# Kernel tuning notes

Hardware: AMD Instinct MI355X
Metric: run time of the kernel (lower is better)

The kernel has to match this reference:

```python
import jax, jax.numpy as jnp
import numpy as np

N_NODES = 10000
N_EDGES = 320000
IN_CH = 128
HID = 64
HEADS = 8
OUT_CH = 2
NEG_SLOPE = 0.2  # PyG GATConv default
EPS = 1e-16      # PyG softmax denominator eps


def setup_inputs() -> dict:
    key = jax.random.key(0)
    ks = jax.random.split(key, 12)
    x = jax.random.normal(ks[0], (N_NODES, IN_CH), dtype=jnp.float32)
    edge_index = jax.random.randint(ks[1], (2, N_EDGES), 0, N_NODES, dtype=jnp.int64)
    s = 0.05
    W1 = jax.random.normal(ks[2], (IN_CH, HEADS * HID), dtype=jnp.float32) * s
    a_src1 = jax.random.normal(ks[3], (HEADS, HID), dtype=jnp.float32) * s
    a_dst1 = jax.random.normal(ks[4], (HEADS, HID), dtype=jnp.float32) * s
    b1 = jnp.zeros((HEADS * HID,), dtype=jnp.float32)
    W2 = jax.random.normal(ks[5], (HEADS * HID, HID), dtype=jnp.float32) * s
    a_src2 = jax.random.normal(ks[6], (1, HID), dtype=jnp.float32) * s
    a_dst2 = jax.random.normal(ks[7], (1, HID), dtype=jnp.float32) * s
    b2 = jnp.zeros((HID,), dtype=jnp.float32)
    Wc = jax.random.normal(ks[8], (HID, OUT_CH), dtype=jnp.float32) * s
    bc = jnp.zeros((OUT_CH,), dtype=jnp.float32)
    return dict(x=x, edge_index=edge_index, W1=W1, a_src1=a_src1, a_dst1=a_dst1,
                b1=b1, W2=W2, a_src2=a_src2, a_dst2=a_dst2, b2=b2, Wc=Wc, bc=bc)


def gat_layer(x, src, dst, W, a_src, a_dst, bias, heads, ch, concat):
    # x: [N, F_in]; src/dst: [E] (self-loops already appended)
    N = x.shape[0]
    h = (x @ W).reshape(N, heads, ch)                 # [N, H, C]
    e_src = jnp.einsum('nhc,hc->nh', h, a_src)        # [N, H]
    e_dst = jnp.einsum('nhc,hc->nh', h, a_dst)
    e = jax.nn.leaky_relu(e_src[src] + e_dst[dst], NEG_SLOPE)  # [E, H]
    # segment softmax over destination nodes (max-shift has zero gradient)
    m = jax.lax.stop_gradient(jax.ops.segment_max(e, dst, num_segments=N))
    w = jnp.exp(e - m[dst])
    denom = jax.ops.segment_sum(w, dst, num_segments=N)
    alpha = w / (denom[dst] + EPS)                    # [E, H]
    # scatter-aggregate weighted source features
    out = jax.ops.segment_sum(h[src] * alpha[:, :, None], dst, num_segments=N)  # [N,H,C]
    out = out.reshape(N, heads * ch) if concat else out.mean(axis=1)
    return out + bias


def reference(x, edge_index, W1, a_src1, a_dst1, b1, W2, a_src2, a_dst2, b2, Wc, bc):
    N = x.shape[0]
    loop = jnp.arange(N, dtype=edge_index.dtype)
    src = jnp.concatenate([edge_index[0], loop])  # PyG add_self_loops=True
    dst = jnp.concatenate([edge_index[1], loop])
    h1 = gat_layer(x, src, dst, W1, a_src1, a_dst1, b1, HEADS, HID, True)
    h1 = jax.nn.elu(h1)
    # dropout is identity in eval mode
    h2 = gat_layer(h1, src, dst, W2, a_src2, a_dst2, b2, 1, HID, False)
    return h2 @ Wc + bc  # [N, 2]
```

## Files before the change

### kernel.cpp

```cpp
#include <hip/hip_runtime.h>
#include <hip/hip_bf16.h>

#define N_NODES 10000
#define N_EDGES 320000
#define IN_CH 128
#define HID 64
#define HEADS 8
#define OUT_CH 2
#define BM 64
#define BCAP 128
#define MPAD 10048
#define AGG1_BLKS 2048
#define AGG2_BLKS 832

typedef __attribute__((ext_vector_type(8))) short frag8;
typedef __attribute__((ext_vector_type(4))) float f32x4;

__device__ __forceinline__ unsigned short f2bf(float f) {
    union { float f; unsigned u; } v; v.f = f;
    unsigned r = (v.u + 0x7FFFu + ((v.u >> 16) & 1u)) >> 16;
    return (unsigned short)r;
}

__device__ __forceinline__ void g2l16(const void* g, void* l) {
    __builtin_amdgcn_global_load_lds(
        (__attribute__((address_space(1))) unsigned int*)g,
        (__attribute__((address_space(3))) unsigned int*)l, 16, 0, 0);
}

__global__ __launch_bounds__(256) void prep_split(
    const float* __restrict__ x, const float* __restrict__ W1,
    const float* __restrict__ W2,
    unsigned short* __restrict__ xh, unsigned short* __restrict__ xl,
    unsigned short* __restrict__ w1h, unsigned short* __restrict__ w1l,
    unsigned short* __restrict__ w2h, unsigned short* __restrict__ w2l,
    int* __restrict__ cursor) {
    int bx = blockIdx.x, tid = threadIdx.x;
    if (bx < 628) {
        int idx = bx * 256 + tid;
        int row = idx >> 4, c = idx & 15;
        float f[8];
        if (row < N_NODES) {
            float4 v0 = *(const float4*)&x[(size_t)row * IN_CH + c * 8];
            float4 v1 = *(const float4*)&x[(size_t)row * IN_CH + c * 8 + 4];
            f[0] = v0.x; f[1] = v0.y; f[2] = v0.z; f[3] = v0.w;
            f[4] = v1.x; f[5] = v1.y; f[6] = v1.z; f[7] = v1.w;
        } else {
            #pragma unroll
            for (int j = 0; j < 8; j++) f[j] = 0.f;
        }
        unsigned short hb[8], lb[8];
        #pragma unroll
        for (int j = 0; j < 8; j++) {
            hb[j] = f2bf(f[j]);
            float hf = __uint_as_float((unsigned)hb[j] << 16);
            lb[j] = f2bf(f[j] - hf);
        }
        size_t o = ((size_t)row * 16 + (c ^ (row & 15))) * 8;
        *(ushort4*)&xh[o]     = make_ushort4(hb[0], hb[1], hb[2], hb[3]);
        *(ushort4*)&xh[o + 4] = make_ushort4(hb[4], hb[5], hb[6], hb[7]);
        *(ushort4*)&xl[o]     = make_ushort4(lb[0], lb[1], lb[2], lb[3]);
        *(ushort4*)&xl[o + 4] = make_ushort4(lb[4], lb[5], lb[6], lb[7]);
    } else if (bx < 660) {
        int idx = (bx - 628) * 256 + tid;
        int kb = idx >> 9, c = idx & 511;
        int hh = c >> 6, cc = c & 63;
        unsigned short hb[8], lb[8];
        #pragma unroll
        for (int i = 0; i < 8; i++) {
            float v = W1[(size_t)(kb * 8 + i) * (HEADS * HID) + c];
            hb[i] = f2bf(v);
            float hf = __uint_as_float((unsigned)hb[i] << 16);
            lb[i] = f2bf(v - hf);
        }
        size_t o = (((size_t)hh * 16 + kb) * 64 + cc) * 8;
        *(ushort4*)&w1h[o]     = make_ushort4(hb[0], hb[1], hb[2], hb[3]);
        *(ushort4*)&w1h[o + 4] = make_ushort4(hb[4], hb[5], hb[6], hb[7]);
        *(ushort4*)&w1l[o]     = make_ushort4(lb[0], lb[1], lb[2], lb[3]);
        *(ushort4*)&w1l[o + 4] = make_ushort4(lb[4], lb[5], lb[6], lb[7]);
    } else if (bx < 676) {
        int idx = (bx - 660) * 256 + tid;
        int kb = idx >> 6, c = idx & 63;
        unsigned short hb[8], lb[8];
        #pragma unroll
        for (int i = 0; i < 8; i++) {
            float v = W2[(size_t)(kb * 8 + i) * 64 + c];
            hb[i] = f2bf(v);
            float hf = __uint_as_float((unsigned)hb[i] << 16);
            lb[i] = f2bf(v - hf);
        }
        size_t o = ((size_t)kb * 64 + c) * 8;
        *(ushort4*)&w2h[o]     = make_ushort4(hb[0], hb[1], hb[2], hb[3]);
        *(ushort4*)&w2h[o + 4] = make_ushort4(hb[4], hb[5], hb[6], hb[7]);
        *(ushort4*)&w2l[o]     = make_ushort4(lb[0], lb[1], lb[2], lb[3]);
        *(ushort4*)&w2l[o + 4] = make_ushort4(lb[4], lb[5], lb[6], lb[7]);
    } else {
        int idx = (bx - 676) * 256 + tid;
        if (idx < 2500) *(int4*)&cursor[idx * 4] = make_int4(0, 0, 0, 0);
    }
}

__global__ __launch_bounds__(256) void gemm1_mfma(
    const unsigned short* __restrict__ xh, const unsigned short* __restrict__ xl,
    const unsigned short* __restrict__ w1h, const unsigned short* __restrict__ w1l,
    const float* __restrict__ a_src1, const float* __restrict__ a_dst1,
    unsigned short* __restrict__ hfeatP,
    float* __restrict__ esAll, float* __restrict__ edAll, int M) {
    __shared__ alignas(16) unsigned short Ah[8192];
    __shared__ alignas(16) unsigned short Al[8192];
    __shared__ alignas(16) unsigned short Bh[8192];
    __shared__ alignas(16) unsigned short Bl[8192];
    int tid = threadIdx.x;
    int lane = tid & 63, w = tid >> 6;
    int vb = (blockIdx.x & 7) * 157 + (blockIdx.x >> 3);
    int h  = vb & 7;
    int bm = (vb >> 3) * BM;

    {
        const unsigned short* gAh = xh  + (size_t)bm * 128;
        const unsigned short* gAl = xl  + (size_t)bm * 128;
        const unsigned short* gBh = w1h + (size_t)h * 8192;
        const unsigned short* gBl = w1l + (size_t)h * 8192;
        #pragma unroll
        for (int i = 0; i < 4; i++) {
            int s = w * 4 + i;
            int go = s * 512 + lane * 8;
            g2l16(gAh + go, &Ah[s * 512]);
            g2l16(gAl + go, &Al[s * 512]);
            g2l16(gBh + go, &Bh[s * 512]);
            g2l16(gBl + go, &Bl[s * 512]);
        }
    }
    __syncthreads();

    int col = lane & 15, g4 = lane >> 4;
    int arow = w * 16 + col;
    f32x4 acc[4] = {};
    #pragma unroll
    for (int ks = 0; ks < 4; ks++) {
        int ai = (arow * 16 + ((ks * 4 + g4) ^ col)) * 8;
        frag8 ah = *(const frag8*)&Ah[ai];
        frag8 al = *(const frag8*)&Al[ai];
        #pragma unroll
        for (int ct = 0; ct < 4; ct++) {
            int bi = ((ks * 4 + g4) * 64 + ct * 16 + col) * 8;
            frag8 bhv = *(const frag8*)&Bh[bi];
            frag8 blv = *(const frag8*)&Bl[bi];
            acc[ct] = __builtin_amdgcn_mfma_f32_16x16x32_bf16(ah, bhv, acc[ct], 0, 0, 0);
            acc[ct] = __builtin_amdgcn_mfma_f32_16x16x32_bf16(al, bhv, acc[ct], 0, 0, 0);
            acc[ct] = __builtin_amdgcn_mfma_f32_16x16x32_bf16(ah, blv, acc[ct], 0, 0, 0);
        }
    }

    float asv[4], adv[4];
    #pragma unroll
    for (int ct = 0; ct < 4; ct++) {
        asv[ct] = a_src1[h * 64 + ct * 16 + col];
        adv[ct] = a_dst1[h * 64 + ct * 16 + col];
    }
    #pragma unroll
    for (int r = 0; r < 4; r++) {
        float s = 0.f, d = 0.f;
        #pragma unroll
        for (int ct = 0; ct < 4; ct++) {
            s += acc[ct][r] * asv[ct];
            d += acc[ct][r] * adv[ct];
        }
        #pragma unroll
        for (int off = 1; off < 16; off <<= 1) {
            s += __shfl_xor(s, off, 64);
            d += __shfl_xor(d, off, 64);
        }
        if (col == 0) {
            int gr = bm + w * 16 + g4 * 4 + r;
            if (gr < M) {
                esAll[(size_t)h * M + gr] = s;
                edAll[(size_t)h * M + gr] = d;
            }
        }
    }

    __syncthreads();
    unsigned short* Tr = Ah;
    int wrow = w * 16 + g4 * 4;
    #pragma unroll
    for (int ct = 0; ct < 4; ct++)
        #pragma unroll
        for (int r = 0; r < 4; r++)
            Tr[(wrow + r) * 68 + ct * 16 + col] = f2bf(acc[ct][r]);
    __syncthreads();
    int row = tid >> 2, q = tid & 3;
    int gr = bm + row;
    if (gr < M) {
        int tb = row * 68 + q * 16;
        ushort4 t0 = *(const ushort4*)&Tr[tb];
        ushort4 t1 = *(const ushort4*)&Tr[tb + 4];
        ushort4 t2 = *(const ushort4*)&Tr[tb + 8];
        ushort4 t3 = *(const ushort4*)&Tr[tb + 12];
        unsigned short* dst =
            &hfeatP[(((size_t)(h >> 1) * M + gr) * 128) + (h & 1) * 64 + q * 16];
        *(ushort4*)&dst[0]  = t0;
        *(ushort4*)&dst[4]  = t1;
        *(ushort4*)&dst[8]  = t2;
        *(ushort4*)&dst[12] = t3;
    }
}

__global__ void fill_bucket(const int* __restrict__ src,
                            const int* __restrict__ dst, int E,
                            int* cursor, int* __restrict__ bucket) {
    int i = blockIdx.x * blockDim.x + threadIdx.x;
    if (i < E) {
        int d = dst[i];
        int pos = atomicAdd(&cursor[d], 1);
        bucket[(d << 7) + min(pos, BCAP - 1)] = src[i];
    }
}

__global__ __launch_bounds__(256) void gemm2_mfma(
    const unsigned short* __restrict__ h1h, const unsigned short* __restrict__ h1l,
    const unsigned short* __restrict__ w2h, const unsigned short* __restrict__ w2l,
    const float* __restrict__ a_src2, const float* __restrict__ a_dst2,
    float* __restrict__ hfeat2, float* __restrict__ es2, float* __restrict__ ed2,
    int M) {
    __shared__ alignas(16) unsigned short Ah[8192];
    __shared__ alignas(16) unsigned short Al[8192];
    __shared__ alignas(16) unsigned short Bh[8192];
    __shared__ alignas(16) unsigned short Bl[8192];
    int tid = threadIdx.x;
    int lane = tid & 63, w = tid >> 6;
    int bm = blockIdx.x * 64;
    int col = lane & 15, g4 = lane >> 4;
    int arow = w * 16 + col;

    f32x4 acc[4] = {};
    for (int t = 0; t < 4; t++) {
        #pragma unroll
        for (int i = 0; i < 4; i++) {
            int s = w * 4 + i;
            int lrow = s * 4 + (lane >> 4);
            int cc = lane & 15;
            int gc = t * 16 + (cc ^ (lrow & 15));
            size_t goA = ((size_t)(bm + lrow) * 64 + gc) * 8;
            g2l16(h1h + goA, &Ah[s * 512]);
            g2l16(h1l + goA, &Al[s * 512]);
            size_t goB = ((size_t)t * 1024 + s * 64 + lane) * 8;
            g2l16(w2h + goB, &Bh[s * 512]);
            g2l16(w2l + goB, &Bl[s * 512]);
        }
        __syncthreads();
        #pragma unroll
        for (int ks = 0; ks < 4; ks++) {
            int ai = (arow * 16 + ((ks * 4 + g4) ^ col)) * 8;
            frag8 ah = *(const frag8*)&Ah[ai];
            frag8 al = *(const frag8*)&Al[ai];
            #pragma unroll
            for (int ct = 0; ct < 4; ct++) {
                int bi = ((ks * 4 + g4) * 64 + ct * 16 + col) * 8;
                frag8 bhv = *(const frag8*)&Bh[bi];
                frag8 blv = *(const frag8*)&Bl[bi];
                acc[ct] = __builtin_amdgcn_mfma_f32_16x16x32_bf16(ah, bhv, acc[ct], 0, 0, 0);
                acc[ct] = __builtin_amdgcn_mfma_f32_16x16x32_bf16(al, bhv, acc[ct], 0, 0, 0);
                acc[ct] = __builtin_amdgcn_mfma_f32_16x16x32_bf16(ah, blv, acc[ct], 0, 0, 0);
            }
        }
        __syncthreads();
    }

    float asv[4], adv[4];
    #pragma unroll
    for (int ct = 0; ct < 4; ct++) {
        asv[ct] = a_src2[ct * 16 + col];
        adv[ct] = a_dst2[ct * 16 + col];
    }
    #pragma unroll
    for (int r = 0; r < 4; r++) {
        int gr = bm + w * 16 + g4 * 4 + r;
        float s = 0.f, d = 0.f;
        #pragma unroll
        for (int ct = 0; ct < 4; ct++) {
            s += acc[ct][r] * asv[ct];
            d += acc[ct][r] * adv[ct];
        }
        #pragma unroll
        for (int off = 1; off < 16; off <<= 1) {
            s += __shfl_xor(s, off, 64);
            d += __shfl_xor(d, off, 64);
        }
        if (gr < M) {
            #pragma unroll
            for (int ct = 0; ct < 4; ct++)
                hfeat2[(size_t)gr * 64 + ct * 16 + col] = acc[ct][r];
            if (col == 0) { es2[gr] = s; ed2[gr] = d; }
        }
    }
}

__global__ __launch_bounds__(256) void gat_agg_pair(
    const unsigned short* __restrict__ hfeatP, const float* __restrict__ esAll,
    const float* __restrict__ edAll, const int* __restrict__ bucket,
    const int* __restrict__ cursor, const float* __restrict__ b1,
    unsigned short* __restrict__ h1h, unsigned short* __restrict__ h1l, int M) {
    __shared__ alignas(16) unsigned rec[4][32][4];
    int bx = blockIdx.x;
    int p = (bx & 7) >> 1;
    int wid = threadIdx.x >> 6;
    int wvp = ((((bx >> 3) << 1) | (bx & 1)) << 2) + wid;
    int l = threadIdx.x & 63;
    int g = l >> 4;
    int q = l & 15;
    int hq = q >> 3;
    int sub = l & 31;
    int hs = l >> 5;
    unsigned (*wrec)[4] = rec[wid];
    const char* hptr = (const char*)hfeatP + (size_t)p * M * 256 + (q << 4);
    const float* esS = esAll + (size_t)(p * 2 + hs) * M;
    const float* edS = edAll + (size_t)(p * 2 + hs) * M;

    for (int n = wvp; n < M; n += 2048) {
        float ednS = edS[n];
        int start = n << 7;
        int deg = min(cursor[n], 96);
        int total = deg + 1;

        float a[8] = {};
        float dloc = 0.f;
        for (int base = 0; base < total; base += 32) {
            int idx = base + sub;
            int sld = bucket[start + idx];
            int sv = (idx < deg) ? sld : n;
            float wgt = 0.f;
            if (idx <= deg) {
                float e = esS[sv] + ednS;
                e = (e > 0.f) ? e : 0.2f * e;
                wgt = __expf(e);
            }
            dloc += wgt;
            if (hs == 0) {
                *(uint2*)&wrec[sub][0] =
                    make_uint2((unsigned)(sv << 8), __float_as_int(wgt));
            } else {
                wrec[sub][2] = __float_as_int(wgt);
            }
            int cnt = min(32, total - base);
            for (int i = 0; i < cnt; i += 4) {
                const uint4 rv = *(const uint4*)&wrec[i + g][0];
                float wg = __uint_as_float(hq ? rv.z : rv.y);
                const uint4 hv = *(const uint4*)(hptr + rv.x);
                a[0] += wg * __uint_as_float(hv.x << 16);
                a[1] += wg * __uint_as_float(hv.x & 0xFFFF0000u);
                a[2] += wg * __uint_as_float(hv.y << 16);
                a[3] += wg * __uint_as_float(hv.y & 0xFFFF0000u);
                a[4] += wg * __uint_as_float(hv.z << 16);
                a[5] += wg * __uint_as_float(hv.z & 0xFFFF0000u);
                a[6] += wg * __uint_as_float(hv.w << 16);
                a[7] += wg * __uint_as_float(hv.w & 0xFFFF0000u);
            }
        }
        #pragma unroll
        for (int off = 16; off; off >>= 1) dloc += __shfl_xor(dloc, off, 64);
        float dother = __shfl_xor(dloc, 32, 64);
        #pragma unroll
        for (int k = 0; k < 8; k++) {
            a[k] += __shfl_xor(a[k], 16, 64);
            a[k] += __shfl_xor(a[k], 32, 64);
        }
        if (g == 0) {
            float d = (hq == 0) ? dloc : dother;
            d += 1e-16f;
            float inv = __builtin_amdgcn_rcpf(d);
            inv = inv * __fmaf_rn(-d, inv, 2.0f);
            const float4 b0v = *(const float4*)&b1[p * 128 + q * 8];
            const float4 b4v = *(const float4*)&b1[p * 128 + q * 8 + 4];
            float vv[8];
            vv[0] = a[0] * inv + b0v.x; vv[1] = a[1] * inv + b0v.y;
            vv[2] = a[2] * inv + b0v.z; vv[3] = a[3] * inv + b0v.w;
            vv[4] = a[4] * inv + b4v.x; vv[5] = a[5] * inv + b4v.y;
            vv[6] = a[6] * inv + b4v.z; vv[7] = a[7] * inv + b4v.w;
            #pragma unroll
            for (int k = 0; k < 8; k++)
                vv[k] = (vv[k] > 0.f) ? vv[k] : (__expf(vv[k]) - 1.f);
            unsigned short hh[8], hl[8];
            #pragma unroll
            for (int k = 0; k < 8; k++) {
                hh[k] = f2bf(vv[k]);
                float hf = __uint_as_float((unsigned)hh[k] << 16);
                hl[k] = f2bf(vv[k] - hf);
            }
            size_t o = ((size_t)n * 64 + p * 16 + q) * 8;
            *(ushort4*)&h1h[o]     = make_ushort4(hh[0], hh[1], hh[2], hh[3]);
            *(ushort4*)&h1h[o + 4] = make_ushort4(hh[4], hh[5], hh[6], hh[7]);
            *(ushort4*)&h1l[o]     = make_ushort4(hl[0], hl[1], hl[2], hl[3]);
            *(ushort4*)&h1l[o + 4] = make_ushort4(hl[4], hl[5], hl[6], hl[7]);
        }
    }
}

__global__ __launch_bounds__(256) void gat_agg2(
    const float* __restrict__ hfeat2, const float* __restrict__ es,
    const float* __restrict__ ed, const int* __restrict__ bucket,
    const int* __restrict__ cursor, const float* __restrict__ b2,
    const float* __restrict__ Wc, const float* __restrict__ bc,
    float* __restrict__ out) {
    __shared__ alignas(8) unsigned rec2[4][64][2];
    int wid = threadIdx.x >> 6;
    int wv = blockIdx.x * 4 + wid;
    int l = threadIdx.x & 63;
    int g = l >> 4;
    int q = l & 15;
    int qoff = q << 4;
    unsigned (*wr2)[2] = rec2[wid];

    for (int n = wv; n < N_NODES; n += AGG2_BLKS * 4) {
        int start = n << 7;
        int deg = min(cursor[n], 96);
        int total = deg + 1;
        float edn = ed[n];

        float ax = 0.f, ay = 0.f, az = 0.f, aw = 0.f;
        float dloc = 0.f;
        for (int base = 0; base < total; base += 64) {
            int cnt = min(64, total - base);
            float wgt = 0.f;
            int sv = n;
            if (l < cnt) {
                int idx = base + l;
                sv = (idx < deg) ? bucket[start + idx] : n;
                float e = es[sv] + edn;
                e = (e > 0.f) ? e : 0.2f * e;
                wgt = __expf(e);
            }
            dloc += wgt;
            *(uint2*)&wr2[l][0] =
                make_uint2((unsigned)(sv << 8), __float_as_int(wgt));
            for (int i = 0; i < cnt; i += 4) {
                const uint2 rv = *(const uint2*)&wr2[i + g][0];
                float wg = __uint_as_float(rv.y);
                const float4 hv =
                    *(const float4*)((const char*)hfeat2 + (rv.x + qoff));
                ax += wg * hv.x;
                ay += wg * hv.y;
                az += wg * hv.z;
                aw += wg * hv.w;
            }
        }
        float d = dloc;
        #pragma unroll
        for (int off = 32; off; off >>= 1) d += __shfl_down(d, off, 64);
        d = __shfl(d, 0, 64) + 1e-16f;
        float inv = __builtin_amdgcn_rcpf(d);
        inv = inv * __fmaf_rn(-d, inv, 2.0f);
        ax += __shfl_down(ax, 32, 64); ay += __shfl_down(ay, 32, 64);
        az += __shfl_down(az, 32, 64); aw += __shfl_down(aw, 32, 64);
        ax += __shfl_down(ax, 16, 64); ay += __shfl_down(ay, 16, 64);
        az += __shfl_down(az, 16, 64); aw += __shfl_down(aw, 16, 64);
        float p0 = 0.f, p1 = 0.f;
        if (g == 0) {
            const float4 bq = *(const float4*)&b2[q * 4];
            float h0 = ax * inv + bq.x, h1v = ay * inv + bq.y;
            float h2v = az * inv + bq.z, h3 = aw * inv + bq.w;
            const float2* WcV = (const float2*)Wc;
            float2 w0 = WcV[q * 4 + 0], w1 = WcV[q * 4 + 1];
            float2 w2 = WcV[q * 4 + 2], w3 = WcV[q * 4 + 3];
            p0 = h0 * w0.x + h1v * w1.x + h2v * w2.x + h3 * w3.x;
            p1 = h0 * w0.y + h1v * w1.y + h2v * w2.y + h3 * w3.y;
        }
        #pragma unroll
        for (int off = 1; off < 16; off <<= 1) {
            p0 += __shfl_xor(p0, off, 64);
            p1 += __shfl_xor(p1, off, 64);
        }
        if (l == 0) {
            out[n * 2 + 0] = p0 + bc[0];
            out[n * 2 + 1] = p1 + bc[1];
        }
    }
}

extern "C" void kernel_launch(void* const* d_in, const int* in_sizes, int n_in,
                              void* d_out, int out_size, void* d_ws, size_t ws_size,
                              hipStream_t stream) {
    const float* x      = (const float*)d_in[0];
    const int*   eidx   = (const int*)d_in[1];
    const float* W1     = (const float*)d_in[2];
    const float* a_src1 = (const float*)d_in[3];
    const float* a_dst1 = (const float*)d_in[4];
    const float* b1     = (const float*)d_in[5];
    const float* W2     = (const float*)d_in[6];
    const float* a_src2 = (const float*)d_in[7];
    const float* a_dst2 = (const float*)d_in[8];
    const float* b2     = (const float*)d_in[9];
    const float* Wc     = (const float*)d_in[10];
    const float* bc     = (const float*)d_in[11];
    float* out = (float*)d_out;

    const int N = N_NODES, E = N_EDGES;
    const int* esrc = eidx;
    const int* edst = eidx + E;

    size_t off = 0;
    auto alloc = [&](size_t bytes) {
        void* p = (char*)d_ws + off;
        off += (bytes + 255) & ~(size_t)255;
        return p;
    };
    int*   cursor   = (int*)alloc((size_t)N * 4);
    int*   bucket   = (int*)alloc((size_t)N * BCAP * 4);
    unsigned short* hfeatP = (unsigned short*)alloc((size_t)4 * N * 128 * 2);
    unsigned short* h1h = (unsigned short*)alloc((size_t)MPAD * 512 * 2);
    unsigned short* h1l = (unsigned short*)alloc((size_t)MPAD * 512 * 2);
    float* hfeat2   = (float*)alloc((size_t)N * 64 * 4);
    float* esAll    = (float*)alloc((size_t)HEADS * N * 4);
    float* edAll    = (float*)alloc((size_t)HEADS * N * 4);
    float* es2      = (float*)alloc((size_t)N * 4);
    float* ed2      = (float*)alloc((size_t)N * 4);
    unsigned short* xh  = (unsigned short*)alloc((size_t)MPAD * 128 * 2);
    unsigned short* xl  = (unsigned short*)alloc((size_t)MPAD * 128 * 2);
    unsigned short* w1h = (unsigned short*)alloc((size_t)128 * 512 * 2);
    unsigned short* w1l = (unsigned short*)alloc((size_t)128 * 512 * 2);
    unsigned short* w2h = (unsigned short*)alloc((size_t)512 * 64 * 2);
    unsigned short* w2l = (unsigned short*)alloc((size_t)512 * 64 * 2);

    prep_split<<<686, 256, 0, stream>>>(x, W1, W2, xh, xl, w1h, w1l, w2h, w2l,
                                        cursor);
    gemm1_mfma<<<157 * 8, 256, 0, stream>>>(xh, xl, w1h, w1l, a_src1, a_dst1,
                                            hfeatP, esAll, edAll, N);
    fill_bucket<<<(E + 255) / 256, 256, 0, stream>>>(esrc, edst, E, cursor, bucket);
    gat_agg_pair<<<AGG1_BLKS, 256, 0, stream>>>(hfeatP, esAll, edAll,
                                                bucket, cursor, b1, h1h, h1l, N);
    gemm2_mfma<<<157, 256, 0, stream>>>(h1h, h1l, w2h, w2l, a_src2, a_dst2,
                                        hfeat2, es2, ed2, N);
    gat_agg2<<<AGG2_BLKS, 256, 0, stream>>>(hfeat2, es2, ed2, bucket, cursor,
                                            b2, Wc, bc, out);
}
```

Measured before the change: 178.8 us.

## Process two nodes per wave and replace LDS edge records with ds_bpermute

The layer-1 aggregation kernel now has each wave handle two destination nodes at once, interleaving their edge gathers so more independent memory loads are in flight. Both aggregation kernels drop the shared-memory record buffer and instead broadcast source offsets and weights across lanes with ds_bpermute. The layer-1 epilogue uses the packed v_cvt_pk_bf16_f32 instruction in place of manual bf16 rounding. The gains come from more memory-level parallelism and less LDS traffic, at the cost of higher register pressure and wasted lanes when the paired nodes differ in degree.

Result: slower. 185.0 us (+3.5%).

```diff
diff --git a/kernel.cpp b/kernel.cpp
--- a/kernel.cpp
+++ b/kernel.cpp
@@ -20,6 +20,12 @@
     union { float f; unsigned u; } v; v.f = f;
     unsigned r = (v.u + 0x7FFFu + ((v.u >> 16) & 1u)) >> 16;
     return (unsigned short)r;
+}
+
+__device__ __forceinline__ unsigned cvt_pk_bf16(float lo, float hi) {
+    unsigned r;
+    asm("v_cvt_pk_bf16_f32 %0, %1, %2" : "=v"(r) : "v"(lo), "v"(hi));
+    return r;
 }
 
 __device__ __forceinline__ void g2l16(const void* g, void* l) {
@@ -296,12 +302,70 @@
     }
 }
 
+#define GATHD(rb, wb, acc) {                                                \
+    int bidx_ = (i << 2) + g4;                                              \
+    int rbg_ = __builtin_amdgcn_ds_bpermute(bidx_, rb);                     \
+    float wg_ = __int_as_float(                                             \
+        __builtin_amdgcn_ds_bpermute(bidx_ + hbaseB, wb));                  \
+    const uint4 hv_ = *(const uint4*)(hptr + rbg_);                         \
+    acc[0] += wg_ * __uint_as_float(hv_.x << 16);                           \
+    acc[1] += wg_ * __uint_as_float(hv_.x & 0xFFFF0000u);                   \
+    acc[2] += wg_ * __uint_as_float(hv_.y << 16);                           \
+    acc[3] += wg_ * __uint_as_float(hv_.y & 0xFFFF0000u);                   \
+    acc[4] += wg_ * __uint_as_float(hv_.z << 16);                           \
+    acc[5] += wg_ * __uint_as_float(hv_.z & 0xFFFF0000u);                   \
+    acc[6] += wg_ * __uint_as_float(hv_.w << 16);                           \
+    acc[7] += wg_ * __uint_as_float(hv_.w & 0xFFFF0000u);                   \
+}
+
+#define STAGE1(stX, degX, ednX, nX, dlX, rbX, wbX) {                        \
+    int idx_ = bse + sub;                                                   \
+    int sld_ = bucket[stX + idx_];                                          \
+    int sv_ = (idx_ < degX) ? sld_ : nX;                                    \
+    float w_ = 0.f;                                                         \
+    if (idx_ <= degX) {                                                     \
+        float e_ = esS[sv_] + ednX;                                         \
+        e_ = (e_ > 0.f) ? e_ : 0.2f * e_;                                   \
+        w_ = __expf(e_);                                                    \
+    }                                                                       \
+    dlX += w_; rbX = sv_ << 8; wbX = __float_as_int(w_);                    \
+}
+
+#define EPIL1(nX, dlX, doX, aX) {                                           \
+    float d_ = (hq == 0) ? dlX : doX;                                       \
+    d_ += 1e-16f;                                                           \
+    float inv_ = __builtin_amdgcn_rcpf(d_);                                 \
+    inv_ = inv_ * __fmaf_rn(-d_, inv_, 2.0f);     \
+    float vv_[8];                                                           \
+    vv_[0] = aX[0] * inv_ + b0v.x; vv_[1] = aX[1] * inv_ + b0v.y;           \
+    vv_[2] = aX[2] * inv_ + b0v.z; vv_[3] = aX[3] * inv_ + b0v.w;           \
+    vv_[4] = aX[4] * inv_ + b4v.x; vv_[5] = aX[5] * inv_ + b4v.y;           \
+    vv_[6] = aX[6] * inv_ + b4v.z; vv_[7] = aX[7] * inv_ + b4v.w;           \
+    _Pragma("unroll")                                                       \
+    for (int k = 0; k < 8; k++)                                             \
+        vv_[k] = (vv_[k] > 0.f) ? vv_[k] : (__expf(vv_[k]) - 1.f);   \
+    unsigned ph0 = cvt_pk_bf16(vv_[0], vv_[1]);                             \
+    unsigned ph1 = cvt_pk_bf16(vv_[2], vv_[3]);                             \
+    unsigned ph2 = cvt_pk_bf16(vv_[4], vv_[5]);                             \
+    unsigned ph3 = cvt_pk_bf16(vv_[6], vv_[7]);                             \
+    unsigned pl0 = cvt_pk_bf16(vv_[0] - __uint_as_float(ph0 << 16),         \
+                               vv_[1] - __uint_as_float(ph0 & 0xFFFF0000u));\
+    unsigned pl1 = cvt_pk_bf16(vv_[2] - __uint_as_float(ph1 << 16),         \
+                               vv_[3] - __uint_as_float(ph1 & 0xFFFF0000u));\
+    unsigned pl2 = cvt_pk_bf16(vv_[4] - __uint_as_float(ph2 << 16),         \
+                               vv_[5] - __uint_as_float(ph2 & 0xFFFF0000u));\
+    unsigned pl3 = cvt_pk_bf16(vv_[6] - __uint_as_float(ph3 << 16),         \
+                               vv_[7] - __uint_as_float(ph3 & 0xFFFF0000u));\
+    size_t o_ = ((size_t)(nX) * 64 + p * 16 + q) * 8;                       \
+    *(uint4*)&h1h[o_] = make_uint4(ph0, ph1, ph2, ph3);                     \
+    *(uint4*)&h1l[o_] = make_uint4(pl0, pl1, pl2, pl3);                     \
+}
+
 __global__ __launch_bounds__(256) void gat_agg_pair(
     const unsigned short* __restrict__ hfeatP, const float* __restrict__ esAll,
     const float* __restrict__ edAll, const int* __restrict__ bucket,
     const int* __restrict__ cursor, const float* __restrict__ b1,
     unsigned short* __restrict__ h1h, unsigned short* __restrict__ h1l, int M) {
-    __shared__ alignas(16) unsigned rec[4][32][4];
     int bx = blockIdx.x;
     int p = (bx & 7) >> 1;
     int wid = threadIdx.x >> 6;
@@ -312,88 +376,65 @@
     int hq = q >> 3;
     int sub = l & 31;
     int hs = l >> 5;
-    unsigned (*wrec)[4] = rec[wid];
+    int g4 = g << 2;
+    int hbaseB = hq << 7;
     const char* hptr = (const char*)hfeatP + (size_t)p * M * 256 + (q << 4);
     const float* esS = esAll + (size_t)(p * 2 + hs) * M;
     const float* edS = edAll + (size_t)(p * 2 + hs) * M;
 
-    for (int n = wvp; n < M; n += 2048) {
-        float ednS = edS[n];
-        int start = n << 7;
-        int deg = min(cursor[n], 96);
-        int total = deg + 1;
-
-        float a[8] = {};
-        float dloc = 0.f;
-        for (int base = 0; base < total; base += 32) {
-            int idx = base + sub;
-            int sld = bucket[start + idx];
-            int sv = (idx < deg) ? sld : n;
-            float wgt = 0.f;
-            if (idx <= deg) {
-                float e = esS[sv] + ednS;
-                e = (e > 0.f) ? e : 0.2f * e;
-                wgt = __expf(e);
+    for (int t = wvp * 2; t < M; t += 4096) {
+        int n0 = t, n1 = t + 1;
+        float edn0 = edS[n0], edn1 = edS[n1];
+        int st0 = n0 << 7, st1 = n1 << 7;
+        int deg0 = min(cursor[n0], 96), deg1 = min(cursor[n1], 96);
+        int tot0 = deg0 + 1, tot1 = deg1 + 1;
+
+        float a0[8] = {}, a1[8] = {};
+        float dl0 = 0.f, dl1 = 0.f;
+        for (int bse = 0; bse < tot0 || bse < tot1; bse += 32) {
+            int c0 = min(32, tot0 - bse);
+            int c1 = min(32, tot1 - bse);
+            int rb0 = 0, wb0 = 0, rb1 = 0, wb1 = 0;
+            if (c0 > 0) STAGE1(st0, deg0, edn0, n0, dl0, rb0, wb0)
+            if (c1 > 0) STAGE1(st1, deg1, edn1, n1, dl1, rb1, wb1)
+            int cm = max(c0, c1);
+            for (int i = 0; i < cm; i += 4) {
+                if (i < c0) GATHD(rb0, wb0, a0)
+                if (i < c1) GATHD(rb1, wb1, a1)
             }
-            dloc += wgt;
-            if (hs == 0) {
-                *(uint2*)&wrec[sub][0] =
-                    make_uint2((unsigned)(sv << 8), __float_as_int(wgt));
-            } else {
-                wrec[sub][2] = __float_as_int(wgt);
-            }
-            int cnt = min(32, total - base);
-            for (int i = 0; i < cnt; i += 4) {
-                const uint4 rv = *(const uint4*)&wrec[i + g][0];
-                float wg = __uint_as_float(hq ? rv.z : rv.y);
-                const uint4 hv = *(const uint4*)(hptr + rv.x);
-                a[0] += wg * __uint_as_float(hv.x << 16);
-                a[1] += wg * __uint_as_float(hv.x & 0xFFFF0000u);
-                a[2] += wg * __uint_as_float(hv.y << 16);
-                a[3] += wg * __uint_as_float(hv.y & 0xFFFF0000u);
-                a[4] += wg * __uint_as_float(hv.z << 16);
-                a[5] += wg * __uint_as_float(hv.z & 0xFFFF0000u);
-                a[6] += wg * __uint_as_float(hv.w << 16);
-                a[7] += wg * __uint_as_float(hv.w & 0xFFFF0000u);
-            }
-        }
-        #pragma unroll
-        for (int off = 16; off; off >>= 1) dloc += __shfl_xor(dloc, off, 64);
-        float dother = __shfl_xor(dloc, 32, 64);
+        }
+        #pragma unroll
+        for (int off = 16; off; off >>= 1) {
+            dl0 += __shfl_xor(dl0, off, 64);
+            dl1 += __shfl_xor(dl1, off, 64);
+        }
+        float do0 = __shfl_xor(dl0, 32, 64);
+        float do1 = __shfl_xor(dl1, 32, 64);
         #pragma unroll
         for (int k = 0; k < 8; k++) {
-            a[k] += __shfl_xor(a[k], 16, 64);
-            a[k] += __shfl_xor(a[k], 32, 64);
+            a0[k] += __shfl_xor(a0[k], 16, 64);
+            a0[k] += __shfl_xor(a0[k], 32, 64);
+            a1[k] += __shfl_xor(a1[k], 16, 64);
+            a1[k] += __shfl_xor(a1[k], 32, 64);
         }
         if (g == 0) {
-            float d = (hq == 0) ? dloc : dother;
-            d += 1e-16f;
-            float inv = __builtin_amdgcn_rcpf(d);
-            inv = inv * __fmaf_rn(-d, inv, 2.0f);
             const float4 b0v = *(const float4*)&b1[p * 128 + q * 8];
             const float4 b4v = *(const float4*)&b1[p * 128 + q * 8 + 4];
-            float vv[8];
-            vv[0] = a[0] * inv + b0v.x; vv[1] = a[1] * inv + b0v.y;
-            vv[2] = a[2] * inv + b0v.z; vv[3] = a[3] * inv + b0v.w;
-            vv[4] = a[4] * inv + b4v.x; vv[5] = a[5] * inv + b4v.y;
-            vv[6] = a[6] * inv + b4v.z; vv[7] = a[7] * inv + b4v.w;
-            #pragma unroll
-            for (int k = 0; k < 8; k++)
-                vv[k] = (vv[k] > 0.f) ? vv[k] : (__expf(vv[k]) - 1.f);
-            unsigned short hh[8], hl[8];
-            #pragma unroll
-            for (int k = 0; k < 8; k++) {
-                hh[k] = f2bf(vv[k]);
-                float hf = __uint_as_float((unsigned)hh[k] << 16);
-                hl[k] = f2bf(vv[k] - hf);
-            }
-            size_t o = ((size_t)n * 64 + p * 16 + q) * 8;
-            *(ushort4*)&h1h[o]     = make_ushort4(hh[0], hh[1], hh[2], hh[3]);
-            *(ushort4*)&h1h[o + 4] = make_ushort4(hh[4], hh[5], hh[6], hh[7]);
-            *(ushort4*)&h1l[o]     = make_ushort4(hl[0], hl[1], hl[2], hl[3]);
-            *(ushort4*)&h1l[o + 4] = make_ushort4(hl[4], hl[5], hl[6], hl[7]);
-        }
-    }
+            EPIL1(n0, dl0, do0, a0)
+            EPIL1(n1, dl1, do1, a1)
+        }
+    }
+}
+
+#define GATH_2(i) {                                                         \
+    int bidx = ((i) << 2) + g4;                                             \
+    int rbg = __builtin_amdgcn_ds_bpermute(bidx, rb);                       \
+    float wg = __int_as_float(__builtin_amdgcn_ds_bpermute(bidx, wb));      \
+    const float4 hv = *(const float4*)((const char*)hfeat2 + (rbg + qoff)); \
+    ax += wg * hv.x;                                                        \
+    ay += wg * hv.y;                                                        \
+    az += wg * hv.z;                                                        \
+    aw += wg * hv.w;                                                        \
 }
 
 __global__ __launch_bounds__(256) void gat_agg2(
@@ -402,14 +443,12 @@
     const int* __restrict__ cursor, const float* __restrict__ b2,
     const float* __restrict__ Wc, const float* __restrict__ bc,
     float* __restrict__ out) {
-    __shared__ alignas(8) unsigned rec2[4][64][2];
-    int wid = threadIdx.x >> 6;
-    int wv = blockIdx.x * 4 + wid;
+    int wv = blockIdx.x * 4 + (threadIdx.x >> 6);
     int l = threadIdx.x & 63;
     int g = l >> 4;
     int q = l & 15;
+    int g4 = g << 2;
     int qoff = q << 4;
-    unsigned (*wr2)[2] = rec2[wid];
 
     for (int n = wv; n < N_NODES; n += AGG2_BLKS * 4) {
         int start = n << 7;
@@ -431,18 +470,9 @@
                 wgt = __expf(e);
             }
             dloc += wgt;
-            *(uint2*)&wr2[l][0] =
-                make_uint2((unsigned)(sv << 8), __float_as_int(wgt));
-            for (int i = 0; i < cnt; i += 4) {
-                const uint2 rv = *(const uint2*)&wr2[i + g][0];
-                float wg = __uint_as_float(rv.y);
-                const float4 hv =
-                    *(const float4*)((const char*)hfeat2 + (rv.x + qoff));
-                ax += wg * hv.x;
-                ay += wg * hv.y;
-                az += wg * hv.z;
-                aw += wg * hv.w;
-            }
+            int rb = sv << 8;
+            int wb = __float_as_int(wgt);
+            for (int i = 0; i < cnt; i += 4) GATH_2(i)
         }
         float d = dloc;
         #pragma unroll
```
